# Optimization experiments

Measured on AMD Instinct MI355X. Metric: run time of the kernel, lower is better.

Reference implementation:

```python
import jax, jax.numpy as jnp
import numpy as np

B, C, T, H, W = 32, 512, 16, 14, 14
DS = 7
HW = H * W
STD = 0.03


def setup_inputs() -> dict:
    key = jax.random.key(0)
    ks = jax.random.split(key, 6)
    x_in = jax.random.normal(ks[0], (B, C, T, HW), jnp.float32)
    # nn.Linear weights stored as (in, out) so forward is x @ W + b
    W1 = jax.random.truncated_normal(ks[1], -2.0, 2.0, (DS * DS * C, C), jnp.float32) * STD
    b1 = jnp.zeros((C,), jnp.float32)
    W2 = jax.random.truncated_normal(ks[2], -2.0, 2.0, (C, C // 8), jnp.float32) * STD
    b2 = jnp.zeros((C // 8,), jnp.float32)
    Wa = jax.random.truncated_normal(ks[3], -2.0, 2.0, (T * T, T // 2), jnp.float32) * STD
    Wd = jax.random.truncated_normal(ks[4], -2.0, 2.0, (T * T, T // 2), jnp.float32) * STD
    return {"x_in": x_in, "W1": W1, "b1": b1, "W2": W2, "b2": b2, "Wa": Wa, "Wd": Wd}


def _temporal_sample(x_in, idx):
    # Faithful to F.grid_sample(bilinear, padding_mode='border', align_corners=False)
    # on a (b, hw*c, t, 1) tensor: the width axis is size 1 and the grid x-coord is 0,
    # which maps exactly to pixel 0 with full weight, so only the t-axis matters.
    # normalize_grid uses n-1 = t-1; unnormalize (align_corners=False) gives:
    #   pixel = ((norm + 1) * t - 1) / 2 = idx * t / (t - 1) - 0.5
    b, c, t, hw = x_in.shape
    p = idx * (t / (t - 1)) - 0.5            # (b, t//2)
    i0 = jnp.floor(p)
    w = (p - i0)[:, None, :, None]           # (b, 1, t//2, 1)
    i0i = i0.astype(jnp.int32)
    i0c = jnp.clip(i0i, 0, t - 1)[:, None, :, None]
    i1c = jnp.clip(i0i + 1, 0, t - 1)[:, None, :, None]
    g0 = jnp.take_along_axis(x_in, jnp.broadcast_to(i0c, (b, c, t // 2, hw)), axis=2)
    g1 = jnp.take_along_axis(x_in, jnp.broadcast_to(i1c, (b, c, t // 2, hw)), axis=2)
    return (1.0 - w) * g0 + w * g1           # (b, c, t//2, hw)


def reference(x_in, W1, b1, W2, b2, Wa, Wd):
    b, c, t, hw = x_in.shape
    # (b, c, t, hw) -> (b, t, c, H, W)
    xi = x_in.reshape(b, c, t, H, W).transpose(0, 2, 1, 3, 4)
    # adaptive_avg_pool2d 14x14 -> 7x7 is an exact 2x2 mean
    xi = xi.reshape(b, t, c, DS, 2, DS, 2).mean(axis=(4, 6))      # (b, t, c, 7, 7)
    xi = xi.transpose(0, 1, 3, 4, 2).reshape(b, t, DS * DS * c)    # (b, t, 25088)
    h = jax.nn.gelu(xi @ W1 + b1, approximate=False)
    feat = h @ W2 + b2                                             # (b, t, c//8)
    scaler = 1.0 / c
    attn = jax.nn.softmax(scaler * jnp.einsum('btd,bsd->bts', feat, feat), axis=-1)
    flat = attn.reshape(b, t * t)
    receptive_field = 2.0
    off_a = jnp.tanh(flat @ Wa) * receptive_field                  # (b, t//2)
    off_d = jnp.tanh(flat @ Wd) * receptive_field
    idx_a = jnp.arange(0, t, 2, dtype=x_in.dtype)[None, :] + off_a
    idx_d = jnp.arange(1, t, 2, dtype=x_in.dtype)[None, :] + off_d
    x_a = _temporal_sample(x_in, idx_a)
    x_d = _temporal_sample(x_in, idx_d)
    return x_a, x_d
```

## Files before the change

kernel.cpp:

```cpp
#include <hip/hip_runtime.h>
#include <math.h>

#define CC 512
#define K1 25088
#define N1 512
#define NE 25690112

typedef unsigned short ushort_t;
typedef __attribute__((ext_vector_type(8))) short bf16x8;
typedef __attribute__((ext_vector_type(4))) float f32x4;
typedef __attribute__((address_space(3))) void* as3_void;
typedef const __attribute__((address_space(1))) void* as1_cvoid;

struct us4 { ushort_t a, b, c, d; };

__device__ __forceinline__ ushort_t f2bf(float f) {
  union { float f; unsigned u; } v; v.f = f;
  unsigned r = v.u + 0x7fffu + ((v.u >> 16) & 1u);
  return (ushort_t)(r >> 16);
}

__device__ __forceinline__ float gelu(float x) {
  return 0.5f * x * (1.0f + erff(x * 0.70710678118654752f));
}

__global__ __launch_bounds__(256)
void k_stage(const float* __restrict__ x, const float* __restrict__ W1,
             ushort_t* __restrict__ A, ushort_t* __restrict__ W1t) {
  __shared__ __align__(16) float smem[64 * 197];
  int tid = threadIdx.x;
  if (blockIdx.x < 3136) {
    float (*tile)[65] = (float (*)[65])smem;
    int u = blockIdx.x;
    int k0 = (u % 392) * 64;
    int n0 = (u / 392) * 64;
    int rg = tid >> 4;
    int m  = tid & 15;
    for (int it = 0; it < 4; ++it) {
      int row = rg + it * 16;
      float4 v = *(const float4*)&W1[(size_t)(k0 + row) * N1 + n0 + m * 4];
      tile[row][m * 4 + 0] = v.x;
      tile[row][m * 4 + 1] = v.y;
      tile[row][m * 4 + 2] = v.z;
      tile[row][m * 4 + 3] = v.w;
    }
    __syncthreads();
    for (int it = 0; it < 4; ++it) {
      int n = rg + it * 16;
      int kb = m * 4;
      us4 o;
      o.a = f2bf(tile[kb + 0][n]);
      o.b = f2bf(tile[kb + 1][n]);
      o.c = f2bf(tile[kb + 2][n]);
      o.d = f2bf(tile[kb + 3][n]);
      *(us4*)&W1t[(size_t)(n0 + n) * K1 + k0 + kb] = o;
    }
  } else {
    float (*s)[197] = (float (*)[197])smem;
    int bx = blockIdx.x - 3136;
    int cch = bx & 7;
    int t = (bx >> 3) & 15;
    int b = bx >> 7;
    int c0 = cch * 64;
    for (int idx = tid; idx < 3136; idx += 256) {
      int c = idx / 49;
      int q = idx - c * 49;
      float4 v = *(const float4*)&x[(((size_t)(b * 512 + c0 + c) * 16) + t) * 196 + q * 4];
      s[c][q * 4 + 0] = v.x;
      s[c][q * 4 + 1] = v.y;
      s[c][q * 4 + 2] = v.z;
      s[c][q * 4 + 3] = v.w;
    }
    __syncthreads();
    ushort_t* dst = A + (size_t)(b * 16 + t) * K1 + c0;
    for (int o = tid; o < 3136; o += 256) {
      int ij = o >> 6;
      int c = o & 63;
      int i = ij / 7;
      int j = ij - i * 7;
      int pos = i * 28 + j * 2;
      float v = (s[c][pos] + s[c][pos + 1] + s[c][pos + 14] + s[c][pos + 15]) * 0.25f;
      dst[ij * 512 + c] = f2bf(v);
    }
  }
}

__global__ __launch_bounds__(256)
void k_gemm1(const ushort_t* __restrict__ A, const ushort_t* __restrict__ Bt,
             float* __restrict__ Cp) {
  __shared__ __align__(16) short As[4][128][8];
  __shared__ __align__(16) short Bs[4][128][8];
  int row0 = blockIdx.x * 128;
  int col0 = blockIdx.y * 128;
  int k0 = blockIdx.z * 512;
  int lane = threadIdx.x & 63;
  int wave = threadIdx.x >> 6;
  int wm = (wave & 1) * 64;
  int wn = (wave >> 1) * 64;
  f32x4 acc[4][4] = {};

  for (int kk = 0; kk < 512; kk += 32) {
    __syncthreads();
    for (int t = 0; t < 2; ++t) {
      int wt = wave * 2 + t;
      int ch = wt >> 1;
      int r0 = (wt & 1) * 64;
      int rr = r0 + lane;
      const ushort_t* ga = A  + (size_t)(row0 + rr) * K1 + (k0 + kk + ch * 8);
      const ushort_t* gb = Bt + (size_t)(col0 + rr) * K1 + (k0 + kk + ch * 8);
      __builtin_amdgcn_global_load_lds((as1_cvoid)ga, (as3_void)&As[ch][r0][0], 16, 0, 0);
      __builtin_amdgcn_global_load_lds((as1_cvoid)gb, (as3_void)&Bs[ch][r0][0], 16, 0, 0);
    }
    __syncthreads();
    int ml = lane & 15, q = lane >> 4;
    bf16x8 af[4], bfr[4];
    for (int sm = 0; sm < 4; ++sm)
      af[sm] = *(const bf16x8*)&As[q][wm + sm * 16 + ml][0];
    for (int sn = 0; sn < 4; ++sn)
      bfr[sn] = *(const bf16x8*)&Bs[q][wn + sn * 16 + ml][0];
    for (int sm = 0; sm < 4; ++sm)
      for (int sn = 0; sn < 4; ++sn)
        acc[sm][sn] = __builtin_amdgcn_mfma_f32_16x16x32_bf16(af[sm], bfr[sn], acc[sm][sn], 0, 0, 0);
  }
  int ml = lane & 15, q = lane >> 4;
  float* out = Cp + (size_t)blockIdx.z * 262144;
  for (int sm = 0; sm < 4; ++sm)
    for (int sn = 0; sn < 4; ++sn)
      for (int rg = 0; rg < 4; ++rg) {
        int row = row0 + wm + sm * 16 + q * 4 + rg;
        int col = col0 + wn + sn * 16 + ml;
        out[row * N1 + col] = acc[sm][sn][rg];
      }
}

__global__ __launch_bounds__(256)
void k_reduce(const float* __restrict__ Cp, const float* __restrict__ b1,
              float* __restrict__ h) {
  int i4 = blockIdx.x * 256 + threadIdx.x;
  const float4* cp4 = (const float4*)Cp;
  float4 a = cp4[i4];
  for (int z = 1; z < 49; ++z) {
    float4 v = cp4[(size_t)z * 65536 + i4];
    a.x += v.x; a.y += v.y; a.z += v.z; a.w += v.w;
  }
  float4 bb = ((const float4*)b1)[i4 & 127];
  float4 r;
  r.x = gelu(a.x + bb.x);
  r.y = gelu(a.y + bb.y);
  r.z = gelu(a.z + bb.z);
  r.w = gelu(a.w + bb.w);
  ((float4*)h)[i4] = r;
}

__global__ __launch_bounds__(512)
void k_head(const float* __restrict__ h, const float* __restrict__ W2,
            const float* __restrict__ b2, const float* __restrict__ Wa,
            const float* __restrict__ Wd, float* __restrict__ offs) {
  int b = blockIdx.x;
  __shared__ float hs[16][512];
  __shared__ float fl[16][65];
  __shared__ float lg[256];
  __shared__ float pr[16][17];
  int tid = threadIdx.x;
  {
    const float4* src = (const float4*)(h + (size_t)b * 8192);
    float4* dst = (float4*)&hs[0][0];
    for (int i = tid; i < 2048; i += 512) dst[i] = src[i];
  }
  __syncthreads();
  {
    int n = tid & 63;
    int tg = tid >> 6;
    float acc0 = 0.f, acc1 = 0.f;
    #pragma unroll 4
    for (int k = 0; k < 512; ++k) {
      float w = W2[k * 64 + n];
      acc0 += hs[tg][k] * w;
      acc1 += hs[tg + 8][k] * w;
    }
    float bias = b2[n];
    fl[tg][n] = acc0 + bias;
    fl[tg + 8][n] = acc1 + bias;
  }
  __syncthreads();
  if (tid < 256) {
    int t = tid >> 4, s = tid & 15;
    float a = 0.f;
    for (int d = 0; d < 64; ++d) a += fl[t][d] * fl[s][d];
    a *= (1.0f / 512.0f);
    float m = a;
    for (int w = 1; w < 16; w <<= 1) m = fmaxf(m, __shfl_xor(m, w, 16));
    float e = expf(a - m);
    float sum = e;
    for (int w = 1; w < 16; w <<= 1) sum += __shfl_xor(sum, w, 16);
    lg[tid] = e / sum;
  }
  __syncthreads();
  if (tid < 256) {
    int o = tid & 15;
    int ch = tid >> 4;
    const float* W = (o >= 8) ? Wd : Wa;
    int col = o & 7;
    float a = 0.f;
    int f0 = ch * 16;
    for (int f = f0; f < f0 + 16; ++f) a += lg[f] * W[f * 8 + col];
    pr[ch][o] = a;
  }
  __syncthreads();
  if (tid < 16) {
    float a = 0.f;
    for (int ch = 0; ch < 16; ++ch) a += pr[ch][tid];
    offs[b * 16 + tid] = tanhf(a) * 2.0f;
  }
}

__global__ __launch_bounds__(256)
void k_sample(const float* __restrict__ x, const float* __restrict__ offs,
              float* __restrict__ out) {
  int bc = blockIdx.x;
  int b = bc >> 9;
  __shared__ float4 xs[16 * 49];
  __shared__ int i0s[16], i1s[16];
  __shared__ float wfr[16];
  int tid = threadIdx.x;
  const float4* src = (const float4*)(x + (size_t)bc * 16 * 196);
  for (int i = tid; i < 784; i += 256) xs[i] = src[i];
  if (tid < 16) {
    int which = tid >> 3, to = tid & 7;
    float idx = (float)(2 * to + which) + offs[b * 16 + tid];
    float p = idx * (16.0f / 15.0f) - 0.5f;
    float fl = floorf(p);
    int i0 = (int)fl;
    wfr[tid] = p - fl;
    i0s[tid] = min(max(i0, 0), 15);
    i1s[tid] = min(max(i0 + 1, 0), 15);
  }
  __syncthreads();
  float4* out4 = (float4*)out;
  for (int oi = tid; oi < 784; oi += 256) {
    int which = oi / 392;
    int rem = oi - which * 392;
    int to = rem / 49;
    int q = rem - to * 49;
    int slot = which * 8 + to;
    float w = wfr[slot];
    float4 g0 = xs[i0s[slot] * 49 + q];
    float4 g1 = xs[i1s[slot] * 49 + q];
    float4 o;
    o.x = g0.x + w * (g1.x - g0.x);
    o.y = g0.y + w * (g1.y - g0.y);
    o.z = g0.z + w * (g1.z - g0.z);
    o.w = g0.w + w * (g1.w - g0.w);
    out4[(size_t)which * (NE / 4) + (size_t)(bc * 8 + to) * 49 + q] = o;
  }
}

extern "C" void kernel_launch(void* const* d_in, const int* in_sizes, int n_in,
                              void* d_out, int out_size, void* d_ws, size_t ws_size,
                              hipStream_t stream) {
  const float* x  = (const float*)d_in[0];
  const float* W1 = (const float*)d_in[1];
  const float* b1 = (const float*)d_in[2];
  const float* W2 = (const float*)d_in[3];
  const float* b2 = (const float*)d_in[4];
  const float* Wa = (const float*)d_in[5];
  const float* Wd = (const float*)d_in[6];
  float* out = (float*)d_out;

  char* w = (char*)d_ws;
  ushort_t* Abf  = (ushort_t*)(w);
  ushort_t* W1t  = (ushort_t*)(w + 25690112);
  float*    Cp   = (float*)(w + 51380224);
  float*    h    = (float*)(w + 51380224 + 51380224);
  float*    offs = (float*)(w + 51380224 + 51380224 + 1048576);

  k_stage<<<7232, 256, 0, stream>>>(x, W1, Abf, W1t);
  k_gemm1<<<dim3(4, 4, 49), 256, 0, stream>>>(Abf, W1t, Cp);
  k_reduce<<<256, 256, 0, stream>>>(Cp, b1, h);
  k_head<<<32, 512, 0, stream>>>(h, W2, b2, Wa, Wd, offs);
  k_sample<<<16384, 256, 0, stream>>>(x, offs, out);
}
```

Before: 551.2 us.

## Double-buffer GEMM1 LDS staging and cut split-K from 49 to 16

The GEMM1 kernel now uses two LDS buffers, so the global-to-LDS load for the next K step is issued before the MFMAs on the current buffer. This replaces the two barriers per iteration with one. Split-K drops from 49 to 16 slices of 1568 K each, which shrinks the partial-sum buffer and the reduce work. In exchange the GEMM launches only 256 blocks on a GPU with many CUs, so occupancy falls and each block runs a longer serial K loop.

After: 554.3 us. About the same (+0.6%).

```diff
diff --git a/kernel.cpp b/kernel.cpp
--- a/kernel.cpp
+++ b/kernel.cpp
@@ -5,6 +5,8 @@
 #define K1 25088
 #define N1 512
 #define NE 25690112
+#define ZSPLIT 16
+#define KPB 1568
 
 typedef unsigned short ushort_t;
 typedef __attribute__((ext_vector_type(8))) short bf16x8;
@@ -88,41 +90,50 @@
 __global__ __launch_bounds__(256)
 void k_gemm1(const ushort_t* __restrict__ A, const ushort_t* __restrict__ Bt,
              float* __restrict__ Cp) {
-  __shared__ __align__(16) short As[4][128][8];
-  __shared__ __align__(16) short Bs[4][128][8];
+  __shared__ __align__(16) short As[2][4][128][8];
+  __shared__ __align__(16) short Bs[2][4][128][8];
   int row0 = blockIdx.x * 128;
   int col0 = blockIdx.y * 128;
-  int k0 = blockIdx.z * 512;
+  int k0 = blockIdx.z * KPB;
   int lane = threadIdx.x & 63;
   int wave = threadIdx.x >> 6;
   int wm = (wave & 1) * 64;
   int wn = (wave >> 1) * 64;
   f32x4 acc[4][4] = {};
 
-  for (int kk = 0; kk < 512; kk += 32) {
-    __syncthreads();
-    for (int t = 0; t < 2; ++t) {
-      int wt = wave * 2 + t;
-      int ch = wt >> 1;
-      int r0 = (wt & 1) * 64;
-      int rr = r0 + lane;
-      const ushort_t* ga = A  + (size_t)(row0 + rr) * K1 + (k0 + kk + ch * 8);
-      const ushort_t* gb = Bt + (size_t)(col0 + rr) * K1 + (k0 + kk + ch * 8);
-      __builtin_amdgcn_global_load_lds((as1_cvoid)ga, (as3_void)&As[ch][r0][0], 16, 0, 0);
-      __builtin_amdgcn_global_load_lds((as1_cvoid)gb, (as3_void)&Bs[ch][r0][0], 16, 0, 0);
-    }
-    __syncthreads();
-    int ml = lane & 15, q = lane >> 4;
+#define STAGE(BUF, KK)                                                          \
+  do {                                                                          \
+    for (int t_ = 0; t_ < 2; ++t_) {                                            \
+      int wt_ = wave * 2 + t_;                                                  \
+      int ch_ = wt_ >> 1;                                                       \
+      int r0_ = (wt_ & 1) * 64;                                                 \
+      int rr_ = r0_ + lane;                                                     \
+      const ushort_t* ga_ = A  + (size_t)(row0 + rr_) * K1 + (k0 + (KK) + ch_ * 8); \
+      const ushort_t* gb_ = Bt + (size_t)(col0 + rr_) * K1 + (k0 + (KK) + ch_ * 8); \
+      __builtin_amdgcn_global_load_lds((as1_cvoid)ga_, (as3_void)&As[BUF][ch_][r0_][0], 16, 0, 0); \
+      __builtin_amdgcn_global_load_lds((as1_cvoid)gb_, (as3_void)&Bs[BUF][ch_][r0_][0], 16, 0, 0); \
+    }                                                                           \
+  } while (0)
+
+  STAGE(0, 0);
+  __syncthreads();
+  int ml = lane & 15, q = lane >> 4;
+  int cur = 0;
+  for (int it = 0; it < 49; ++it) {
+    if (it < 48) STAGE(cur ^ 1, (it + 1) * 32);
     bf16x8 af[4], bfr[4];
     for (int sm = 0; sm < 4; ++sm)
-      af[sm] = *(const bf16x8*)&As[q][wm + sm * 16 + ml][0];
+      af[sm] = *(const bf16x8*)&As[cur][q][wm + sm * 16 + ml][0];
     for (int sn = 0; sn < 4; ++sn)
-      bfr[sn] = *(const bf16x8*)&Bs[q][wn + sn * 16 + ml][0];
+      bfr[sn] = *(const bf16x8*)&Bs[cur][q][wn + sn * 16 + ml][0];
     for (int sm = 0; sm < 4; ++sm)
       for (int sn = 0; sn < 4; ++sn)
         acc[sm][sn] = __builtin_amdgcn_mfma_f32_16x16x32_bf16(af[sm], bfr[sn], acc[sm][sn], 0, 0, 0);
-  }
-  int ml = lane & 15, q = lane >> 4;
+    __syncthreads();
+    cur ^= 1;
+  }
+#undef STAGE
+
   float* out = Cp + (size_t)blockIdx.z * 262144;
   for (int sm = 0; sm < 4; ++sm)
     for (int sn = 0; sn < 4; ++sn)
@@ -139,7 +150,7 @@
   int i4 = blockIdx.x * 256 + threadIdx.x;
   const float4* cp4 = (const float4*)Cp;
   float4 a = cp4[i4];
-  for (int z = 1; z < 49; ++z) {
+  for (int z = 1; z < ZSPLIT; ++z) {
     float4 v = cp4[(size_t)z * 65536 + i4];
     a.x += v.x; a.y += v.y; a.z += v.z; a.w += v.w;
   }
@@ -271,11 +282,11 @@
   ushort_t* Abf  = (ushort_t*)(w);
   ushort_t* W1t  = (ushort_t*)(w + 25690112);
   float*    Cp   = (float*)(w + 51380224);
-  float*    h    = (float*)(w + 51380224 + 51380224);
-  float*    offs = (float*)(w + 51380224 + 51380224 + 1048576);
+  float*    h    = (float*)(w + 51380224 + 16777216);
+  float*    offs = (float*)(w + 51380224 + 16777216 + 1048576);
 
   k_stage<<<7232, 256, 0, stream>>>(x, W1, Abf, W1t);
-  k_gemm1<<<dim3(4, 4, 49), 256, 0, stream>>>(Abf, W1t, Cp);
+  k_gemm1<<<dim3(4, 4, ZSPLIT), 256, 0, stream>>>(Abf, W1t, Cp);
   k_reduce<<<256, 256, 0, stream>>>(Cp, b1, h);
   k_head<<<32, 512, 0, stream>>>(h, W2, b2, Wa, Wd, offs);
   k_sample<<<16384, 256, 0, stream>>>(x, offs, out);
```
